# Kernel tuning notes

Measured on AMD Instinct MI355X. Metric: run time of the kernel, lower is better.

Reference implementation:

```python
import jax, jax.numpy as jnp
import numpy as np
from jax import lax

NUM_SEGMENTS = 50
HIDDEN = 128
IN_CH = 64
LOGSIG_DIM = IN_CH + IN_CH * (IN_CH - 1) // 2 + IN_CH  # level1 + Levy area + startpoint


def setup_inputs() -> dict:
    key = jax.random.key(0)
    k0, k1, k2, k3, k4 = jax.random.split(key, 5)
    B, C, T, V = 16, IN_CH, 200, 25
    x = jax.random.normal(k0, (B, C, T, V), dtype=jnp.float32)
    s = 1.0 / np.sqrt(HIDDEN).astype(np.float32)
    W_ih = jax.random.uniform(k1, (4 * HIDDEN, LOGSIG_DIM), jnp.float32, -s, s)
    W_hh = jax.random.uniform(k2, (4 * HIDDEN, HIDDEN), jnp.float32, -s, s)
    b_ih = jax.random.uniform(k3, (4 * HIDDEN,), jnp.float32, -s, s)
    b_hh = jax.random.uniform(k4, (4 * HIDDEN,), jnp.float32, -s, s)
    return {"x": x, "W_ih": W_ih, "W_hh": W_hh, "b_ih": b_ih, "b_hh": b_hh}


def _segment_logsig(xn):
    # xn: (N, C, T). Split T into NUM_SEGMENTS chunks; level-2 log-signature per chunk.
    N, C, T = xn.shape
    L = T // NUM_SEGMENTS  # points per segment
    p = xn.transpose(0, 2, 1).reshape(N, NUM_SEGMENTS, L, C)  # path points
    start = p[:, :, 0]                                  # (N,S,C) segment startpoint
    inc = p[:, :, 1:] - p[:, :, :-1]                    # (N,S,L-1,C) increments
    dev = p[:, :, :-1] - start[:, :, None]              # (N,S,L-1,C) p_t - p_0
    # Level-2 iterated integrals (cross terms): S2_ij = sum_t dev_t,i * inc_t,j
    S2 = jnp.einsum('nsti,nstj->nsij', dev, inc)        # (N,S,C,C)
    A = 0.5 * (S2 - S2.transpose(0, 1, 3, 2))           # Levy area (antisymmetric part)
    iu, ju = jnp.triu_indices(C, k=1)
    levy = A[:, :, iu, ju]                              # (N,S,C(C-1)/2)
    lvl1 = p[:, :, -1] - start                          # (N,S,C) level-1 term
    return jnp.concatenate([lvl1, levy, start], axis=-1)  # (N,S,LOGSIG_DIM)


def _lstm(seq, W_ih, W_hh, b_ih, b_hh):
    # seq: (N, S, F). Single-layer unidirectional LSTM, torch gate order (i,f,g,o).
    N = seq.shape[0]
    x_proj = jnp.einsum('nsf,gf->nsg', seq, W_ih) + b_ih + b_hh  # (N,S,4H)

    def step(carry, xt):
        h, c = carry
        gates = xt + h @ W_hh.T
        i, f, g, o = jnp.split(gates, 4, axis=-1)
        c = jax.nn.sigmoid(f) * c + jax.nn.sigmoid(i) * jnp.tanh(g)
        h = jax.nn.sigmoid(o) * jnp.tanh(c)
        return (h, c), h

    h0 = jnp.zeros((N, HIDDEN), seq.dtype)
    c0 = jnp.zeros((N, HIDDEN), seq.dtype)
    _, hs = lax.scan(step, (h0, c0), x_proj.transpose(1, 0, 2))
    return hs.transpose(1, 0, 2)  # (N,S,H)


def reference(x, W_ih, W_hh, b_ih, b_hh):
    B, C, T, V = x.shape
    xn = x.transpose(0, 3, 1, 2).reshape(B * V, C, T)
    ls = _segment_logsig(xn)                      # (B*V, S, LOGSIG_DIM)
    h = _lstm(ls, W_ih, W_hh, b_ih, b_hh)          # (B*V, S, H)
    out = h.reshape(B, V, NUM_SEGMENTS, HIDDEN).transpose(0, 3, 2, 1)
    return out  # (B, H, S, V)
```

## Files before the change

### kernel.cpp

```cpp
#include <hip/hip_runtime.h>
#include <stdint.h>

#define NSEG 50
#define HID 128
#define KDIM 2144
#define KD2 2176
#define KD2B 4352
#define NROW 20000
#define NROW_PAD 20096
#define GATES 512
#define NSEQ 400

typedef __attribute__((ext_vector_type(8))) _Float16 f16x8;
typedef __attribute__((ext_vector_type(4))) float f32x4;
typedef __attribute__((ext_vector_type(4))) uint32_t u32x4;

#define GLB_SPACE __attribute__((address_space(1)))
#define LDS_SPACE __attribute__((address_space(3)))

__device__ __forceinline__ void g2lds16(const void* g, void* l) {
    __builtin_amdgcn_global_load_lds((const GLB_SPACE uint32_t*)g,
                                     (LDS_SPACE uint32_t*)l, 16, 0, 0);
}

__global__ __launch_bounds__(256) void feat_kernel(const float* __restrict__ x,
                                                   const float* __restrict__ Wih,
                                                   const float* __restrict__ Whh,
                                                   const float* __restrict__ bih,
                                                   const float* __restrict__ bhh,
                                                   _Float16* __restrict__ feat,
                                                   _Float16* __restrict__ wh,
                                                   _Float16* __restrict__ whh16,
                                                   float* __restrict__ bias) {
    int bid = blockIdx.x;
    int tid = threadIdx.x;

    if (bid >= 800) {
        const int nwih = 512 * KD2;
        const int nwhh = 512 * HID;
        const int total = nwih + nwhh + 512;
        for (int idx = (bid - 800) * 256 + tid; idx < total; idx += 64 * 256) {
            if (idx < nwih) {
                int row = idx / KD2;
                int k = idx - row * KD2;
                wh[idx] = (k < KDIM) ? (_Float16)Wih[row * KDIM + k] : (_Float16)0.0f;
            } else if (idx < nwih + nwhh) {
                int q = idx - nwih;
                whh16[q] = (_Float16)Whh[q];
            } else {
                int g = idx - nwih - nwhh;
                bias[g] = bih[g] + bhh[g];
            }
        }
        return;
    }

    int b = bid / NSEG;
    int s = bid - b * NSEG;

    __shared__ float pbuf[64 * 100];
    __shared__ __align__(16) float4 uv4[25 * 64];

    for (int i = tid; i < 6400; i += 256) {
        int c = i / 100;
        int r = i - c * 100;
        pbuf[c * 100 + r] = x[(((size_t)b * 64 + c) * 200 + 4 * s) * 25 + r];
    }
    if (tid < 800) {
        int v = tid >> 5;
        int k = 2144 + (tid & 31);
        size_t m = ((size_t)(b * 25 + v)) * NSEG + s;
        feat[m * KD2 + k] = (_Float16)0.0f;
    }
    __syncthreads();

    for (int i = tid; i < 1600; i += 256) {
        int v = i >> 6;
        int c = i & 63;
        float p0 = pbuf[c * 100 + v];
        float p1 = pbuf[c * 100 + 25 + v];
        float p2 = pbuf[c * 100 + 50 + v];
        float p3 = pbuf[c * 100 + 75 + v];
        uv4[v * 64 + c] = make_float4(p1 - p0, p2 - p0, p2 - p1, p3 - p2);
        size_t m = ((size_t)(b * 25 + v)) * NSEG + s;
        feat[m * KD2 + c] = (_Float16)(p3 - p0);
        feat[m * KD2 + 2080 + c] = (_Float16)p0;
    }
    __syncthreads();

    for (int ch = 0; ch < 8; ch++) {
        int pidx = ch * 256 + tid;
        if (pidx < 2016) {
            float disc = 16129.0f - 8.0f * (float)pidx;
            int i = (int)((127.0f - sqrtf(disc)) * 0.5f);
            int off = 63 * i - (i * (i - 1)) / 2;
            while (off > pidx) { i--; off = 63 * i - (i * (i - 1)) / 2; }
            while (63 * (i + 1) - ((i + 1) * i) / 2 <= pidx) { i++; off = 63 * i - (i * (i - 1)) / 2; }
            int j = pidx - off + i + 1;
            int k = 64 + pidx;
            for (int v = 0; v < 25; v++) {
                float4 a = uv4[v * 64 + i];
                float4 bb = uv4[v * 64 + j];
                float val = 0.5f * (a.x * bb.z - bb.x * a.z + a.y * bb.w - bb.y * a.w);
                size_t m = ((size_t)(b * 25 + v)) * NSEG + s;
                feat[m * KD2 + k] = (_Float16)val;
            }
        }
    }
}

__global__ __launch_bounds__(128, 2) void gemm_kernel(const _Float16* __restrict__ feat,
                                                      const _Float16* __restrict__ wh,
                                                      const float* __restrict__ bias,
                                                      _Float16* __restrict__ xproj2) {
    int bid = blockIdx.x;
    int x = bid & 7;
    int t = bid >> 3;
    int nb = t & 3;
    int mt = (t >> 2) * 8 + x;
    if (mt >= 157) return;
    int m0 = mt * 128;
    int n0 = nb * 128;
    int tid = threadIdx.x;
    int wave = tid >> 6;
    int lane = tid & 63;
    int quad = lane >> 4;
    int l15 = lane & 15;
    int wm = wave * 64;

    int r8 = lane >> 3;
    int gcol = ((lane & 7) * 16) ^ (r8 * 16);

    __shared__ __align__(16) _Float16 smem[16896];
    char* As = (char*)smem;
    char* Bs = (char*)smem + 128 * 128;

    const f32x4 z4 = {0.f, 0.f, 0.f, 0.f};
    f32x4 acc[4][8];
    for (int i = 0; i < 4; i++)
        for (int j = 0; j < 8; j++) acc[i][j] = z4;

    const char* featB = (const char*)feat;
    const char* whB = (const char*)wh;

    for (int kt = 0; kt < 34; kt++) {
        size_t kb = (size_t)kt * 128;
        __syncthreads();
        for (int it = 0; it < 8; it++) {
            int rb = it * 16 + wave * 8;
            g2lds16(featB + (size_t)(m0 + rb + r8) * KD2B + kb + gcol, As + rb * 128);
            g2lds16(whB + (size_t)(n0 + rb + r8) * KD2B + kb + gcol, Bs + rb * 128);
        }
        __syncthreads();

        for (int ks = 0; ks < 2; ks++) {
            int off = ((ks * 64) | (quad * 16)) ^ ((l15 & 7) * 16);
            f16x8 af[4], bf[8];
            for (int tt = 0; tt < 4; tt++)
                af[tt] = *(const f16x8*)(As + (wm + tt * 16 + l15) * 128 + off);
            for (int tt = 0; tt < 8; tt++)
                bf[tt] = *(const f16x8*)(Bs + (tt * 16 + l15) * 128 + off);
            for (int mtl = 0; mtl < 4; mtl++)
                for (int ntl = 0; ntl < 8; ntl++)
                    acc[mtl][ntl] = __builtin_amdgcn_mfma_f32_16x16x32_f16(af[mtl], bf[ntl], acc[mtl][ntl], 0, 0, 0);
        }
    }

    __syncthreads();
    for (int ntl = 0; ntl < 8; ntl++) {
        int nl = ntl * 16 + l15;
        float bv = bias[n0 + nl];
        for (int mtl = 0; mtl < 4; mtl++)
            for (int r = 0; r < 4; r++) {
                int ml = wm + mtl * 16 + quad * 4 + r;
                smem[ml * 132 + nl] = (_Float16)(acc[mtl][ntl][r] + bv);
            }
    }
    __syncthreads();
    {
        int row = tid;
        int m = m0 + row;
        if (m < NROW) {
            unsigned q = (unsigned)m / 50u;
            unsigned s = (unsigned)m - q * 50u;
            const char* src = (const char*)smem + row * 264;
            char* dst = (char*)xproj2 + ((size_t)s * NSEQ + q) * 1024 + (size_t)n0 * 2;
            for (int i = 0; i < 16; i++)
                *(u32x4*)(dst + i * 16) = *(const u32x4*)(src + i * 16);
        }
    }
}

__global__ __launch_bounds__(512, 2) void lstm_kernel(const _Float16* __restrict__ xproj2,
                                                      const _Float16* __restrict__ whh,
                                                      _Float16* __restrict__ hseq) {
    int bid = blockIdx.x;
    int tid = threadIdx.x;
    int wave = tid >> 6;
    int lane = tid & 63;
    int quad = lane >> 4;
    int col = lane & 15;
    int hid = wave * 16 + col;

    __shared__ __align__(16) char xbuf[25 * 4 * 1040];
    __shared__ __align__(16) _Float16 hst[NSEG * 4 * HID];
    __shared__ __align__(16) _Float16 hbuf[2][4 * 144];

    f16x8 bfrag[4][4];
    for (int g = 0; g < 4; g++) {
        int n = g * 128 + hid;
        for (int kq = 0; kq < 4; kq++)
            bfrag[g][kq] = *(const f16x8*)(whh + (size_t)n * HID + kq * 32 + quad * 8);
    }
    for (int i = tid; i < 2 * 4 * 144; i += 512) ((_Float16*)hbuf)[i] = (_Float16)0.0f;
    float cst = 0.0f;

    const char* xsrc = (const char*)xproj2;
    for (int r = wave; r < 100; r += 8)
        g2lds16(xsrc + ((size_t)((r >> 2) * NSEQ + bid * 4 + (r & 3))) * 1024 + lane * 16,
                xbuf + r * 1040);
    __syncthreads();

    const f32x4 z4 = {0.f, 0.f, 0.f, 0.f};
    for (int half = 0; half < 2; half++) {
        for (int ss = 0; ss < 25; ss++) {
            int s = half * 25 + ss;
            int cur = s & 1;
            int nxt = cur ^ 1;

            f16x8 afrag[4];
            for (int kq = 0; kq < 4; kq++)
                afrag[kq] = *(const f16x8*)(&hbuf[cur][(col & 3) * 144 + kq * 32 + quad * 8]);

            float xp[4];
            for (int g = 0; g < 4; g++)
                xp[g] = (float)(*(const _Float16*)(xbuf + (ss * 4 + quad) * 1040 +
                               (g * 128 + hid) * 2));

            f32x4 acc[4];
            for (int g = 0; g < 4; g++) {
                acc[g] = z4;
                for (int kq = 0; kq < 4; kq++)
                    acc[g] = __builtin_amdgcn_mfma_f32_16x16x32_f16(afrag[kq], bfrag[g][kq], acc[g], 0, 0, 0);
            }

            float gv[4];
            for (int g = 0; g < 4; g++) {
                float lo = (quad & 1) ? acc[g][1] : acc[g][0];
                float hi = (quad & 1) ? acc[g][3] : acc[g][2];
                gv[g] = (quad & 2) ? hi : lo;
            }

            float ip = gv[0] + xp[0];
            float fp = gv[1] + xp[1];
            float gp = gv[2] + xp[2];
            float op = gv[3] + xp[3];
            float si = __fdividef(1.0f, 1.0f + __expf(-ip));
            float sf = __fdividef(1.0f, 1.0f + __expf(-fp));
            float so = __fdividef(1.0f, 1.0f + __expf(-op));
            float eg = __expf(-2.0f * gp);
            float tg = __fdividef(1.0f - eg, 1.0f + eg);
            cst = sf * cst + si * tg;
            float ec = __expf(-2.0f * cst);
            float tc = __fdividef(1.0f - ec, 1.0f + ec);
            float hv = so * tc;
            _Float16 hv16 = (_Float16)hv;
            hbuf[nxt][quad * 144 + hid] = hv16;
            hst[(s * 4 + quad) * 128 + hid] = hv16;
            __syncthreads();
        }
        if (half == 0) {
            for (int r = wave; r < 100; r += 8)
                g2lds16(xsrc + ((size_t)((25 + (r >> 2)) * NSEQ + bid * 4 + (r & 3))) * 1024 + lane * 16,
                        xbuf + r * 1040);
            __syncthreads();
        }
    }

    const u32x4* src = (const u32x4*)hst;
    for (int i = tid; i < 3200; i += 512) {
        int s = i >> 6;
        int rem = i & 63;
        int seq = rem >> 4;
        int seg = rem & 15;
        u32x4 v = src[i];
        *(u32x4*)((char*)hseq + ((size_t)(s * NSEQ + bid * 4 + seq)) * 256 + seg * 16) = v;
    }
}

__global__ __launch_bounds__(256) void tr_kernel(const _Float16* __restrict__ hseq,
                                                 float* __restrict__ out) {
    int bid = blockIdx.x;
    int b = bid / NSEG;
    int s = bid - b * NSEG;
    int tid = threadIdx.x;

    __shared__ _Float16 buf[25 * 130];

    const uint32_t* src32 = (const uint32_t*)(hseq + ((size_t)s * NSEQ + b * 25) * HID);
    uint32_t* buf32 = (uint32_t*)buf;
    for (int i = tid; i < 1600; i += 256) {
        int v = i >> 6;
        int d = i & 63;
        buf32[v * 65 + d] = src32[i];
    }
    __syncthreads();
    for (int i = tid; i < 3200; i += 256) {
        int hid = i / 25;
        int v = i - hid * 25;
        out[(((size_t)b * 128 + hid) * NSEG + s) * 25 + v] = (float)buf[v * 130 + hid];
    }
}

extern "C" void kernel_launch(void* const* d_in, const int* in_sizes, int n_in,
                              void* d_out, int out_size, void* d_ws, size_t ws_size,
                              hipStream_t stream) {
    const float* x = (const float*)d_in[0];
    const float* Wih = (const float*)d_in[1];
    const float* Whh = (const float*)d_in[2];
    const float* bih = (const float*)d_in[3];
    const float* bhh = (const float*)d_in[4];
    float* out = (float*)d_out;

    char* ws = (char*)d_ws;
    size_t off = 0;
    _Float16* feat = (_Float16*)(ws + off);   off += (size_t)NROW_PAD * KD2 * 2;
    _Float16* xproj2 = (_Float16*)(ws + off); off += (size_t)NSEG * NSEQ * GATES * 2;
    _Float16* hseq = (_Float16*)(ws + off);   off += (size_t)NSEG * NSEQ * HID * 2;
    _Float16* wh = (_Float16*)(ws + off);     off += (size_t)512 * KD2 * 2;
    _Float16* whh16 = (_Float16*)(ws + off);  off += (size_t)512 * HID * 2;
    float* bias = (float*)(ws + off);         off += 512 * 4;

    hipLaunchKernelGGL(feat_kernel, dim3(864), dim3(256), 0, stream,
                       x, Wih, Whh, bih, bhh, feat, wh, whh16, bias);
    hipLaunchKernelGGL(gemm_kernel, dim3(640), dim3(128), 0, stream, feat, wh, bias, xproj2);
    hipLaunchKernelGGL(lstm_kernel, dim3(100), dim3(512), 0, stream, xproj2, whh16, hseq);
    hipLaunchKernelGGL(tr_kernel, dim3(16 * NSEG), dim3(256), 0, stream, hseq, out);
}
```

Measured before the change: 220.7 us.

## Regroup Levy-area features into 4-wide runs and split GEMM tile across four waves

Reorders the Levy-area feature columns so that each thread computes four consecutive j-values for a fixed i and writes them as one 8-byte vector store, padding K to 2240. A matching column permutation is applied to W_ih during weight conversion, with zeros in the padded slots. The feature kernel moves to 512 threads with padded LDS strides to reduce bank conflicts. The GEMM now uses 256 threads, each wave owning a 64x64 subtile instead of 64x128, which lowers register pressure and raises occupancy, at the cost of one extra K iteration.

```diff
diff --git a/kernel.cpp b/kernel.cpp
--- a/kernel.cpp
+++ b/kernel.cpp
@@ -4,14 +4,16 @@
 #define NSEG 50
 #define HID 128
 #define KDIM 2144
-#define KD2 2176
-#define KD2B 4352
+#define KD2 2240
+#define KD2B 4480
 #define NROW 20000
 #define NROW_PAD 20096
 #define GATES 512
 #define NSEQ 400
+#define NGRP 528
 
 typedef __attribute__((ext_vector_type(8))) _Float16 f16x8;
+typedef __attribute__((ext_vector_type(4))) _Float16 f16x4;
 typedef __attribute__((ext_vector_type(4))) float f32x4;
 typedef __attribute__((ext_vector_type(4))) uint32_t u32x4;
 
@@ -23,7 +25,23 @@
                                      (LDS_SPACE uint32_t*)l, 16, 0, 0);
 }
 
-__global__ __launch_bounds__(256) void feat_kernel(const float* __restrict__ x,
+__device__ __forceinline__ int goff528(int i) {
+    int n = 63 - i;
+    int q = n >> 2, t = n & 3;
+    return NGRP - (q + 1) * (2 * q + t);
+}
+__device__ __forceinline__ int ifromg(int g) {
+    int i = 63 - (int)sqrtf(8.0f * (float)(NGRP - g));
+    if (i < 0) i = 0;
+    if (i > 62) i = 62;
+    while (i > 0 && goff528(i) > g) i--;
+    while (goff528(i + 1) <= g) i++;
+    return i;
+}
+
+#define UVP(c) ((((c) & 3) << 4) | ((c) >> 2))
+
+__global__ __launch_bounds__(512) void feat_kernel(const float* __restrict__ x,
                                                    const float* __restrict__ Wih,
                                                    const float* __restrict__ Whh,
                                                    const float* __restrict__ bih,
@@ -35,15 +53,35 @@
     int bid = blockIdx.x;
     int tid = threadIdx.x;
 
+    __shared__ float pbuf[64 * 101];
+    __shared__ __align__(16) float4 uv4[25 * 64];
+
     if (bid >= 800) {
+        int* kmap = (int*)pbuf;
+        for (int k = tid; k < KD2; k += 512) {
+            int orig;
+            if (k < 64) {
+                orig = k;
+            } else if (k < 64 + 4 * NGRP) {
+                int g = (k - 64) >> 2, p = (k - 64) & 3;
+                int i = ifromg(g);
+                int j = i + 1 + 4 * (g - goff528(i)) + p;
+                orig = (j < 64) ? (64 + 63 * i - (i * (i - 1)) / 2 + (j - i - 1)) : -1;
+            } else {
+                orig = 2080 + (k - (64 + 4 * NGRP));
+            }
+            kmap[k] = orig;
+        }
+        __syncthreads();
         const int nwih = 512 * KD2;
         const int nwhh = 512 * HID;
         const int total = nwih + nwhh + 512;
-        for (int idx = (bid - 800) * 256 + tid; idx < total; idx += 64 * 256) {
+        for (int idx = (bid - 800) * 512 + tid; idx < total; idx += 64 * 512) {
             if (idx < nwih) {
                 int row = idx / KD2;
                 int k = idx - row * KD2;
-                wh[idx] = (k < KDIM) ? (_Float16)Wih[row * KDIM + k] : (_Float16)0.0f;
+                int orig = kmap[k];
+                wh[idx] = (orig >= 0) ? (_Float16)Wih[row * KDIM + orig] : (_Float16)0.0f;
             } else if (idx < nwih + nwhh) {
                 int q = idx - nwih;
                 whh16[q] = (_Float16)Whh[q];
@@ -58,58 +96,58 @@
     int b = bid / NSEG;
     int s = bid - b * NSEG;
 
-    __shared__ float pbuf[64 * 100];
-    __shared__ __align__(16) float4 uv4[25 * 64];
-
-    for (int i = tid; i < 6400; i += 256) {
+    for (int i = tid; i < 6400; i += 512) {
         int c = i / 100;
         int r = i - c * 100;
-        pbuf[c * 100 + r] = x[(((size_t)b * 64 + c) * 200 + 4 * s) * 25 + r];
-    }
-    if (tid < 800) {
-        int v = tid >> 5;
-        int k = 2144 + (tid & 31);
-        size_t m = ((size_t)(b * 25 + v)) * NSEG + s;
-        feat[m * KD2 + k] = (_Float16)0.0f;
-    }
-    __syncthreads();
-
-    for (int i = tid; i < 1600; i += 256) {
+        pbuf[c * 101 + r] = x[(((size_t)b * 64 + c) * 200 + 4 * s) * 25 + r];
+    }
+    __syncthreads();
+
+    for (int i = tid; i < 1600; i += 512) {
         int v = i >> 6;
         int c = i & 63;
-        float p0 = pbuf[c * 100 + v];
-        float p1 = pbuf[c * 100 + 25 + v];
-        float p2 = pbuf[c * 100 + 50 + v];
-        float p3 = pbuf[c * 100 + 75 + v];
-        uv4[v * 64 + c] = make_float4(p1 - p0, p2 - p0, p2 - p1, p3 - p2);
+        float p0 = pbuf[c * 101 + v];
+        float p1 = pbuf[c * 101 + 25 + v];
+        float p2 = pbuf[c * 101 + 50 + v];
+        float p3 = pbuf[c * 101 + 75 + v];
+        uv4[v * 64 + UVP(c)] = make_float4(p1 - p0, p2 - p0, p2 - p1, p3 - p2);
         size_t m = ((size_t)(b * 25 + v)) * NSEG + s;
         feat[m * KD2 + c] = (_Float16)(p3 - p0);
-        feat[m * KD2 + 2080 + c] = (_Float16)p0;
-    }
-    __syncthreads();
-
-    for (int ch = 0; ch < 8; ch++) {
-        int pidx = ch * 256 + tid;
-        if (pidx < 2016) {
-            float disc = 16129.0f - 8.0f * (float)pidx;
-            int i = (int)((127.0f - sqrtf(disc)) * 0.5f);
-            int off = 63 * i - (i * (i - 1)) / 2;
-            while (off > pidx) { i--; off = 63 * i - (i * (i - 1)) / 2; }
-            while (63 * (i + 1) - ((i + 1) * i) / 2 <= pidx) { i++; off = 63 * i - (i * (i - 1)) / 2; }
-            int j = pidx - off + i + 1;
-            int k = 64 + pidx;
-            for (int v = 0; v < 25; v++) {
-                float4 a = uv4[v * 64 + i];
-                float4 bb = uv4[v * 64 + j];
-                float val = 0.5f * (a.x * bb.z - bb.x * a.z + a.y * bb.w - bb.y * a.w);
-                size_t m = ((size_t)(b * 25 + v)) * NSEG + s;
-                feat[m * KD2 + k] = (_Float16)val;
-            }
-        }
-    }
-}
-
-__global__ __launch_bounds__(128, 2) void gemm_kernel(const _Float16* __restrict__ feat,
+        feat[m * KD2 + (64 + 4 * NGRP) + c] = (_Float16)p0;
+    }
+    __syncthreads();
+
+    for (int g = tid; g < NGRP; g += 512) {
+        int i = ifromg(g);
+        int t = g - goff528(i);
+        int j0 = i + 1 + 4 * t;
+        int k0 = 64 + 4 * g;
+        float msk[4];
+        int jc[4];
+#pragma unroll
+        for (int p = 0; p < 4; p++) {
+            int j = j0 + p;
+            msk[p] = (j < 64) ? 0.5f : 0.0f;
+            jc[p] = (j < 64) ? UVP(j) : UVP(63);
+        }
+        int ip = UVP(i);
+        for (int v = 0; v < 25; v++) {
+            const float4* rowv = &uv4[v * 64];
+            float4 a = rowv[ip];
+            f16x4 o;
+#pragma unroll
+            for (int p = 0; p < 4; p++) {
+                float4 bb = rowv[jc[p]];
+                float val = msk[p] * (a.x * bb.z - bb.x * a.z + a.y * bb.w - bb.y * a.w);
+                o[p] = (_Float16)val;
+            }
+            size_t m = ((size_t)(b * 25 + v)) * NSEG + s;
+            *(f16x4*)(feat + m * KD2 + k0) = o;
+        }
+    }
+}
+
+__global__ __launch_bounds__(256, 4) void gemm_kernel(const _Float16* __restrict__ feat,
                                                       const _Float16* __restrict__ wh,
                                                       const float* __restrict__ bias,
                                                       _Float16* __restrict__ xproj2) {
@@ -126,7 +164,8 @@
     int lane = tid & 63;
     int quad = lane >> 4;
     int l15 = lane & 15;
-    int wm = wave * 64;
+    int wm = (wave >> 1) * 64;
+    int wn = (wave & 1) * 64;
 
     int r8 = lane >> 3;
     int gcol = ((lane & 7) * 16) ^ (r8 * 16);
@@ -136,18 +175,18 @@
     char* Bs = (char*)smem + 128 * 128;
 
     const f32x4 z4 = {0.f, 0.f, 0.f, 0.f};
-    f32x4 acc[4][8];
+    f32x4 acc[4][4];
     for (int i = 0; i < 4; i++)
-        for (int j = 0; j < 8; j++) acc[i][j] = z4;
+        for (int j = 0; j < 4; j++) acc[i][j] = z4;
 
     const char* featB = (const char*)feat;
     const char* whB = (const char*)wh;
 
-    for (int kt = 0; kt < 34; kt++) {
+    for (int kt = 0; kt < 35; kt++) {
         size_t kb = (size_t)kt * 128;
         __syncthreads();
-        for (int it = 0; it < 8; it++) {
-            int rb = it * 16 + wave * 8;
+        for (int it = 0; it < 4; it++) {
+            int rb = it * 32 + wave * 8;
             g2lds16(featB + (size_t)(m0 + rb + r8) * KD2B + kb + gcol, As + rb * 128);
             g2lds16(whB + (size_t)(n0 + rb + r8) * KD2B + kb + gcol, Bs + rb * 128);
         }
@@ -155,20 +194,20 @@
 
         for (int ks = 0; ks < 2; ks++) {
             int off = ((ks * 64) | (quad * 16)) ^ ((l15 & 7) * 16);
-            f16x8 af[4], bf[8];
+            f16x8 af[4], bf[4];
             for (int tt = 0; tt < 4; tt++)
                 af[tt] = *(const f16x8*)(As + (wm + tt * 16 + l15) * 128 + off);
-            for (int tt = 0; tt < 8; tt++)
-                bf[tt] = *(const f16x8*)(Bs + (tt * 16 + l15) * 128 + off);
+            for (int tt = 0; tt < 4; tt++)
+                bf[tt] = *(const f16x8*)(Bs + (wn + tt * 16 + l15) * 128 + off);
             for (int mtl = 0; mtl < 4; mtl++)
-                for (int ntl = 0; ntl < 8; ntl++)
+                for (int ntl = 0; ntl < 4; ntl++)
                     acc[mtl][ntl] = __builtin_amdgcn_mfma_f32_16x16x32_f16(af[mtl], bf[ntl], acc[mtl][ntl], 0, 0, 0);
         }
     }
 
     __syncthreads();
-    for (int ntl = 0; ntl < 8; ntl++) {
-        int nl = ntl * 16 + l15;
+    for (int ntl = 0; ntl < 4; ntl++) {
+        int nl = wn + ntl * 16 + l15;
         float bv = bias[n0 + nl];
         for (int mtl = 0; mtl < 4; mtl++)
             for (int r = 0; r < 4; r++) {
@@ -178,14 +217,15 @@
     }
     __syncthreads();
     {
-        int row = tid;
+        int row = tid >> 1;
+        int half = tid & 1;
         int m = m0 + row;
         if (m < NROW) {
             unsigned q = (unsigned)m / 50u;
             unsigned s = (unsigned)m - q * 50u;
-            const char* src = (const char*)smem + row * 264;
-            char* dst = (char*)xproj2 + ((size_t)s * NSEQ + q) * 1024 + (size_t)n0 * 2;
-            for (int i = 0; i < 16; i++)
+            const char* src = (const char*)smem + row * 264 + half * 128;
+            char* dst = (char*)xproj2 + ((size_t)s * NSEQ + q) * 1024 + (size_t)n0 * 2 + half * 128;
+            for (int i = 0; i < 8; i++)
                 *(u32x4*)(dst + i * 16) = *(const u32x4*)(src + i * 16);
         }
     }
@@ -331,9 +371,9 @@
     _Float16* whh16 = (_Float16*)(ws + off);  off += (size_t)512 * HID * 2;
     float* bias = (float*)(ws + off);         off += 512 * 4;
 
-    hipLaunchKernelGGL(feat_kernel, dim3(864), dim3(256), 0, stream,
+    hipLaunchKernelGGL(feat_kernel, dim3(864), dim3(512), 0, stream,
                        x, Wih, Whh, bih, bhh, feat, wh, whh16, bias);
-    hipLaunchKernelGGL(gemm_kernel, dim3(640), dim3(128), 0, stream, feat, wh, bias, xproj2);
+    hipLaunchKernelGGL(gemm_kernel, dim3(640), dim3(256), 0, stream, feat, wh, bias, xproj2);
     hipLaunchKernelGGL(lstm_kernel, dim3(100), dim3(512), 0, stream, xproj2, whh16, hseq);
     hipLaunchKernelGGL(tr_kernel, dim3(16 * NSEG), dim3(256), 0, stream, hseq, out);
 }
```

Result: faster. 212.7 us (-3.6%).
